# Performance work log

Hardware: AMD Instinct MI355X
Metric: run time of the kernel (lower is better)

## Reference

```python
import jax, jax.numpy as jnp
import numpy as np

B, T, D = 4, 2048, 1024
H, HD = 16, 64  # num_heads, head_size; H*HD == D
DFF = 4 * D
EPS = 1e-5

def _ln(x, g, b):
    mu = jnp.mean(x, axis=-1, keepdims=True)
    var = jnp.mean(jnp.square(x - mu), axis=-1, keepdims=True)
    return (x - mu) * jax.lax.rsqrt(var + EPS) * g + b

def setup_inputs() -> dict:
    key = jax.random.key(0)
    ks = jax.random.split(key, 12)
    s = lambda fan_in: 1.0 / np.sqrt(fan_in)
    return {
        "x": jax.random.normal(ks[0], (B, T, D), jnp.float32),
        "Wq": jax.random.normal(ks[1], (H, D, HD), jnp.float32) * s(D),
        "Wk": jax.random.normal(ks[2], (H, D, HD), jnp.float32) * s(D),
        "Wv": jax.random.normal(ks[3], (H, D, HD), jnp.float32) * s(D),
        "Wo": jax.random.normal(ks[4], (D, D), jnp.float32) * s(D),
        "bo": jax.random.normal(ks[5], (D,), jnp.float32) * 0.01,
        "W1": jax.random.normal(ks[6], (D, DFF), jnp.float32) * s(D),
        "b1": jax.random.normal(ks[7], (DFF,), jnp.float32) * 0.01,
        "W2": jax.random.normal(ks[8], (DFF, D), jnp.float32) * s(DFF),
        "b2": jax.random.normal(ks[9], (D,), jnp.float32) * 0.01,
        "g1": jnp.ones((D,), jnp.float32),
        "be1": jnp.zeros((D,), jnp.float32),
        "g2": jnp.ones((D,), jnp.float32),
        "be2": jnp.zeros((D,), jnp.float32),
    }

def reference(x, Wq, Wk, Wv, Wo, bo, W1, b1, W2, b2, g1, be1, g2, be2):
    # pre-LN attention
    h = _ln(x, g1, be1)                                   # [B,T,D]
    q = jnp.einsum('btd,hde->bhte', h, Wq)                # [B,H,T,HD]
    k = jnp.einsum('btd,hde->bhte', h, Wk)
    v = jnp.einsum('btd,hde->bhte', h, Wv)
    scores = jnp.einsum('bhte,bhse->bhts', q, k) * (HD ** -0.5)  # [B,H,T,T]
    mask = jnp.tril(jnp.ones((T, T), bool))
    scores = jnp.where(mask, scores, -jnp.inf)
    attn = jax.nn.softmax(scores, axis=-1)
    ctx = jnp.einsum('bhts,bhse->bhte', attn, v)          # [B,H,T,HD]
    ctx = ctx.transpose(0, 2, 1, 3).reshape(B, T, D)      # concat heads
    x = x + jnp.einsum('btd,de->bte', ctx, Wo) + bo
    # pre-LN FFN
    h2 = _ln(x, g2, be2)
    ff = jax.nn.relu(jnp.einsum('btd,df->btf', h2, W1) + b1)
    x = x + jnp.einsum('btf,fd->btd', ff, W2) + b2
    return x
```

## Files before the change

### kernel.cpp

```cpp
#include <hip/hip_runtime.h>
#include <stdint.h>

#define B_ 4
#define T_ 2048
#define D_ 1024
#define H_ 16
#define HD_ 64
#define DFF_ 4096
#define M_ (B_ * T_)

typedef __bf16 bf16x8 __attribute__((ext_vector_type(8)));
typedef float f32x4 __attribute__((ext_vector_type(4)));

__device__ __forceinline__ uint16_t f2bf(float f) {
  union { float f; uint32_t u; } v;
  v.f = f;
  uint32_t r = v.u + 0x7FFF + ((v.u >> 16) & 1);
  return (uint16_t)(r >> 16);
}

#define GLD_LDS(gp, lp)                                                        \
  __builtin_amdgcn_global_load_lds(                                            \
      (const __attribute__((address_space(1))) void*)(gp),                     \
      (__attribute__((address_space(3))) void*)(lp), 16, 0, 0)

__global__ __launch_bounds__(256) void ln_bf16(const float* __restrict__ x,
                                               const float* __restrict__ gamma,
                                               const float* __restrict__ beta,
                                               uint16_t* __restrict__ out) {
  __shared__ float red[4];
  const int tid = threadIdx.x;
  const size_t row = blockIdx.x;
  const float4 v = ((const float4*)(x + row * D_))[tid];
  float s = v.x + v.y + v.z + v.w;
#pragma unroll
  for (int off = 32; off >= 1; off >>= 1) s += __shfl_xor(s, off, 64);
  if ((tid & 63) == 0) red[tid >> 6] = s;
  __syncthreads();
  const float mean = (red[0] + red[1] + red[2] + red[3]) * (1.0f / D_);
  const float d0 = v.x - mean, d1 = v.y - mean, d2 = v.z - mean, d3 = v.w - mean;
  float ss = d0 * d0 + d1 * d1 + d2 * d2 + d3 * d3;
#pragma unroll
  for (int off = 32; off >= 1; off >>= 1) ss += __shfl_xor(ss, off, 64);
  __syncthreads();
  if ((tid & 63) == 0) red[tid >> 6] = ss;
  __syncthreads();
  const float var = (red[0] + red[1] + red[2] + red[3]) * (1.0f / D_);
  const float rstd = rsqrtf(var + 1e-5f);
  const float4 g = ((const float4*)gamma)[tid];
  const float4 b = ((const float4*)beta)[tid];
  ushort4 o;
  o.x = f2bf(d0 * rstd * g.x + b.x);
  o.y = f2bf(d1 * rstd * g.y + b.y);
  o.z = f2bf(d2 * rstd * g.z + b.z);
  o.w = f2bf(d3 * rstd * g.w + b.w);
  ((ushort4*)(out + row * D_))[tid] = o;
}

__global__ __launch_bounds__(256) void prep_weights(
    const float* __restrict__ Wq, const float* __restrict__ Wk,
    const float* __restrict__ Wv, const float* __restrict__ Wo,
    const float* __restrict__ W1, const float* __restrict__ W2,
    uint16_t* __restrict__ wqkvt, uint16_t* __restrict__ wot,
    uint16_t* __restrict__ w1t, uint16_t* __restrict__ w2t) {
  __shared__ float tile[32][33];
  const int tx = threadIdx.x & 31, ty = threadIdx.x >> 5;
  const int pid = blockIdx.x;

  if (pid >= 9216) {
    const int p = pid - 9216;
    const int bx = p & 1, by = (p >> 1) & 31, z = p >> 6;
    const int which = z >> 4, hh = z & 15;
    const float* W = (which == 0) ? Wq : ((which == 1) ? Wk : Wv);
    const float* in = W + (size_t)hh * D_ * HD_;
    const int e0 = bx * 32, d0 = by * 32;
#pragma unroll
    for (int i = 0; i < 32; i += 8)
      tile[ty + i][tx] = in[(size_t)(d0 + ty + i) * HD_ + e0 + tx];
    __syncthreads();
#pragma unroll
    for (int i = 0; i < 32; i += 8)
      wqkvt[((size_t)(which * 1024 + hh * 64) + e0 + ty + i) * D_ + d0 + tx] =
          f2bf(tile[tx][ty + i]);
    return;
  }

  const float* in;
  uint16_t* out;
  int R, C, bx, by;
  if (pid < 1024) {
    in = Wo; out = wot; R = 1024; C = 1024; bx = pid & 31; by = pid >> 5;
  } else if (pid < 5120) {
    const int p = pid - 1024;
    in = W1; out = w1t; R = 1024; C = 4096; bx = p & 127; by = p >> 7;
  } else {
    const int p = pid - 5120;
    in = W2; out = w2t; R = 4096; C = 1024; bx = p & 31; by = p >> 5;
  }
  const int c0 = bx * 32, r0 = by * 32;
#pragma unroll
  for (int i = 0; i < 32; i += 8)
    tile[ty + i][tx] = in[(size_t)(r0 + ty + i) * C + c0 + tx];
  __syncthreads();
#pragma unroll
  for (int i = 0; i < 32; i += 8)
    out[(size_t)(c0 + ty + i) * R + r0 + tx] = f2bf(tile[tx][ty + i]);
}

template <int BN>
__global__ __launch_bounds__(256) void gemm_bf16(const uint16_t* __restrict__ A,
                                                 const uint16_t* __restrict__ Bt,
                                                 void* __restrict__ C,
                                                 const float* __restrict__ bias,
                                                 const float* __restrict__ resid,
                                                 int M, int N, int K, int lda,
                                                 int ldb, int flags) {
  constexpr int NJ = BN / 32;
  __shared__ __align__(16) uint16_t As[128 * 64];
  __shared__ __align__(16) uint16_t Bs[BN * 64];
  const int tid = threadIdx.x;
  const int lane = tid & 63, w = tid >> 6;
  const int quad = lane >> 4, lr = lane & 15;
  const int wr = w >> 1, wc = w & 1;

  const int n_tiles = N / BN;
  const int pid = blockIdx.x;
  const int grp = 16 * n_tiles;
  const int gid = pid / grp;
  const int rem = pid - gid * grp;
  const int nt = rem / 16;
  const int mt = gid * 16 + (rem - nt * 16);
  const int bn0 = nt * BN, bm0 = mt * 128;

  f32x4 acc[4][NJ];
#pragma unroll
  for (int i = 0; i < 4; i++)
#pragma unroll
    for (int j = 0; j < NJ; j++) acc[i][j] = f32x4{0.f, 0.f, 0.f, 0.f};

  const int s_row = lane >> 3, s_slot = lane & 7;

  for (int k0 = 0; k0 < K; k0 += 64) {
#pragma unroll
    for (int u = 0; u < 4; u++) {
      const int r = w * 32 + u * 8 + s_row;
      const int cg = s_slot ^ (r & 7);
      GLD_LDS(A + (size_t)(bm0 + r) * lda + k0 + cg * 8, As + (w * 32 + u * 8) * 64);
    }
#pragma unroll
    for (int u = 0; u < NJ; u++) {
      const int r = w * (BN / 4) + u * 8 + s_row;
      const int cg = s_slot ^ (r & 7);
      GLD_LDS(Bt + (size_t)(bn0 + r) * ldb + k0 + cg * 8,
              Bs + (w * (BN / 4) + u * 8) * 64);
    }
    __syncthreads();

#pragma unroll
    for (int ks = 0; ks < 2; ks++) {
      bf16x8 af[4], bfr[NJ];
#pragma unroll
      for (int i = 0; i < 4; i++) {
        const int m = wr * 64 + i * 16 + lr;
        const int slot = (ks * 4 + quad) ^ (m & 7);
        af[i] = *(const bf16x8*)(As + m * 64 + slot * 8);
      }
#pragma unroll
      for (int j = 0; j < NJ; j++) {
        const int n = wc * (BN / 2) + j * 16 + lr;
        const int slot = (ks * 4 + quad) ^ (n & 7);
        bfr[j] = *(const bf16x8*)(Bs + n * 64 + slot * 8);
      }
#pragma unroll
      for (int i = 0; i < 4; i++)
#pragma unroll
        for (int j = 0; j < NJ; j++)
          acc[i][j] =
              __builtin_amdgcn_mfma_f32_16x16x32_bf16(af[i], bfr[j], acc[i][j], 0, 0, 0);
    }
    __syncthreads();
  }

  const int base_m = bm0 + wr * 64 + quad * 4;
  const int base_n = bn0 + wc * (BN / 2) + lr;
#pragma unroll
  for (int i = 0; i < 4; i++) {
#pragma unroll
    for (int j = 0; j < NJ; j++) {
      const int col = base_n + j * 16;
      const float bv = bias ? bias[col] : 0.f;
#pragma unroll
      for (int r = 0; r < 4; r++) {
        const size_t row = base_m + i * 16 + r;
        float v = acc[i][j][r] + bv;
        if (resid) v += resid[row * N + col];
        if (flags & 1) v = fmaxf(v, 0.f);
        if (flags & 2)
          ((uint16_t*)C)[row * N + col] = f2bf(v);
        else
          ((float*)C)[row * N + col] = v;
      }
    }
  }
}

__global__ __launch_bounds__(256) void v_transpose(const uint16_t* __restrict__ qkv,
                                                   uint16_t* __restrict__ vtb) {
  __shared__ __align__(16) uint16_t tile[64 * 72];
  const int tid = threadIdx.x;
  const int t0 = blockIdx.x * 64;
  const int bh = blockIdx.y;
  const int b = bh >> 4, h = bh & 15;
  const uint16_t* src = qkv + (size_t)b * T_ * 3072 + 2048 + h * 64;
#pragma unroll
  for (int u = 0; u < 2; u++) {
    const int uu = tid + u * 256;
    const int r = uu >> 3, c = uu & 7;
    *(int4*)(tile + r * 72 + c * 8) =
        *(const int4*)(src + (size_t)(t0 + r) * 3072 + c * 8);
  }
  __syncthreads();
  uint16_t* dst = vtb + ((size_t)bh * 64) * T_ + t0;
#pragma unroll
  for (int u = 0; u < 2; u++) {
    const int uu = tid + u * 256;
    const int e = uu >> 3, c2 = uu & 7;
    union { uint16_t u16[8]; int4 v; } tmp;
#pragma unroll
    for (int jj = 0; jj < 8; jj++) tmp.u16[jj] = tile[(c2 * 8 + jj) * 72 + e];
    *(int4*)(dst + (size_t)e * T_ + c2 * 8) = tmp.v;
  }
}

__global__ __launch_bounds__(256) void attn_mfma(const uint16_t* __restrict__ qkv,
                                                 const uint16_t* __restrict__ vtb,
                                                 uint16_t* __restrict__ ctx) {
  __shared__ __align__(16) uint16_t Ks[2][64 * 64];
  __shared__ __align__(16) uint16_t Vt[2][64 * 64];
  __shared__ __align__(16) uint16_t Ps[128 * 72];
  const int tid = threadIdx.x;
  const int lane = tid & 63, w = tid >> 6;
  const int quad = lane >> 4, lr = lane & 15;
  const int lr7 = lr & 7;
  const int h = blockIdx.y, b = blockIdx.z;
  const uint16_t* base = qkv + (size_t)b * T_ * 3072 + h * 64;
  const uint16_t* vbase = vtb + ((size_t)(b * H_ + h) * 64) * T_;
  const int s_row = lane >> 3, s_slot = lane & 7;

#pragma unroll
  for (int half = 0; half < 2; half++) {
    const int tq = (half == 0) ? (int)blockIdx.x : 15 - (int)blockIdx.x;
    const int q0 = tq * 128;

    bf16x8 aq[2][2];
#pragma unroll
    for (int i = 0; i < 2; i++)
#pragma unroll
      for (int ks = 0; ks < 2; ks++)
        aq[i][ks] = *(const bf16x8*)(base + (size_t)(q0 + w * 32 + i * 16 + lr) * 3072 +
                                     ks * 32 + quad * 8);

    f32x4 oacc[2][4];
#pragma unroll
    for (int i = 0; i < 2; i++)
#pragma unroll
      for (int j = 0; j < 4; j++) oacc[i][j] = f32x4{0.f, 0.f, 0.f, 0.f};
    float l_part[2] = {0.f, 0.f};

    const int row_min_w = q0 + w * 32;
    const int row_max_w = row_min_w + 31;
    const int nstg = 2 * tq + 2;

    __syncthreads();
#pragma unroll
    for (int u = 0; u < 2; u++) {
      const int r = w * 16 + u * 8 + s_row;
      const int cg = s_slot ^ (r & 7);
      GLD_LDS(base + 1024 + (size_t)r * 3072 + cg * 8, Ks[0] + (w * 16 + u * 8) * 64);
      GLD_LDS(vbase + (size_t)r * T_ + cg * 8, Vt[0] + (w * 16 + u * 8) * 64);
    }

    for (int st = 0; st < nstg; st++) {
      __syncthreads();
      if (st + 1 < nstg) {
        uint16_t* Kb = Ks[(st + 1) & 1];
        uint16_t* Vb = Vt[(st + 1) & 1];
#pragma unroll
        for (int u = 0; u < 2; u++) {
          const int r = w * 16 + u * 8 + s_row;
          const int cg = s_slot ^ (r & 7);
          GLD_LDS(base + 1024 + (size_t)((st + 1) * 64 + r) * 3072 + cg * 8,
                  Kb + (w * 16 + u * 8) * 64);
          GLD_LDS(vbase + (size_t)r * T_ + (st + 1) * 64 + cg * 8,
                  Vb + (w * 16 + u * 8) * 64);
        }
      }

      if (st * 64 > row_max_w) continue;
      const uint16_t* Kb = Ks[st & 1];
      const uint16_t* Vb = Vt[st & 1];

      f32x4 sa[2][4];
#pragma unroll
      for (int i = 0; i < 2; i++)
#pragma unroll
        for (int sf = 0; sf < 4; sf++) sa[i][sf] = f32x4{0.f, 0.f, 0.f, 0.f};
#pragma unroll
      for (int ks = 0; ks < 2; ks++) {
        bf16x8 ak[4];
#pragma unroll
        for (int sf = 0; sf < 4; sf++) {
          const int slot = (ks * 4 + quad) ^ lr7;
          ak[sf] = *(const bf16x8*)(Kb + (sf * 16 + lr) * 64 + slot * 8);
        }
#pragma unroll
        for (int i = 0; i < 2; i++)
#pragma unroll
          for (int sf = 0; sf < 4; sf++)
            sa[i][sf] = __builtin_amdgcn_mfma_f32_16x16x32_bf16(ak[sf], aq[i][ks],
                                                                sa[i][sf], 0, 0, 0);
      }

      const bool diag = (st * 64 + 63 > row_min_w);
      if (diag) {
#pragma unroll
        for (int i = 0; i < 2; i++) {
          const int mrow = q0 + w * 32 + i * 16 + lr;
#pragma unroll
          for (int sf = 0; sf < 4; sf++) {
            const int s0 = st * 64 + sf * 16 + quad * 4;
            float p[4];
#pragma unroll
            for (int r = 0; r < 4; r++) {
              float sv = sa[i][sf][r];
              if (s0 + r > mrow) sv = -1e30f;
              p[r] = exp2f(fmaf(sv, 0.18033688f, -28.8539008f));
              l_part[i] += p[r];
            }
            ushort4 pk;
            pk.x = f2bf(p[0]);
            pk.y = f2bf(p[1]);
            pk.z = f2bf(p[2]);
            pk.w = f2bf(p[3]);
            *(ushort4*)(Ps + (size_t)(w * 32 + i * 16 + lr) * 72 + sf * 16 + quad * 4) =
                pk;
          }
        }
      } else {
#pragma unroll
        for (int i = 0; i < 2; i++) {
#pragma unroll
          for (int sf = 0; sf < 4; sf++) {
            float p[4];
#pragma unroll
            for (int r = 0; r < 4; r++) {
              p[r] = exp2f(fmaf(sa[i][sf][r], 0.18033688f, -28.8539008f));
              l_part[i] += p[r];
            }
            ushort4 pk;
            pk.x = f2bf(p[0]);
            pk.y = f2bf(p[1]);
            pk.z = f2bf(p[2]);
            pk.w = f2bf(p[3]);
            *(ushort4*)(Ps + (size_t)(w * 32 + i * 16 + lr) * 72 + sf * 16 + quad * 4) =
                pk;
          }
        }
      }

#pragma unroll
      for (int ks = 0; ks < 2; ks++) {
        bf16x8 ap[2], bv[4];
#pragma unroll
        for (int i = 0; i < 2; i++)
          ap[i] = *(const bf16x8*)(Ps + (size_t)(w * 32 + i * 16 + lr) * 72 + ks * 32 +
                                   quad * 8);
#pragma unroll
        for (int j = 0; j < 4; j++) {
          const int slot = (ks * 4 + quad) ^ lr7;
          bv[j] = *(const bf16x8*)(Vb + (j * 16 + lr) * 64 + slot * 8);
        }
#pragma unroll
        for (int i = 0; i < 2; i++)
#pragma unroll
          for (int j = 0; j < 4; j++)
            oacc[i][j] =
                __builtin_amdgcn_mfma_f32_16x16x32_bf16(ap[i], bv[j], oacc[i][j], 0, 0, 0);
      }
    }

    float linv[2];
#pragma unroll
    for (int i = 0; i < 2; i++) {
      float l = l_part[i];
      l += __shfl_xor(l, 16, 64);
      l += __shfl_xor(l, 32, 64);
      linv[i] = 1.f / l;
    }
    uint16_t* ob =
        ctx + ((size_t)b * T_ + q0 + w * 32 + quad * 4) * D_ + h * 64 + lr;
#pragma unroll
    for (int i = 0; i < 2; i++)
#pragma unroll
      for (int r = 0; r < 4; r++) {
        const float inv = __shfl(linv[i], quad * 4 + r, 64);
#pragma unroll
        for (int j = 0; j < 4; j++)
          ob[(size_t)(i * 16 + r) * D_ + j * 16] = f2bf(oacc[i][j][r] * inv);
      }
  }
}

extern "C" void kernel_launch(void* const* d_in, const int* in_sizes, int n_in,
                              void* d_out, int out_size, void* d_ws, size_t ws_size,
                              hipStream_t stream) {
  const float* x = (const float*)d_in[0];
  const float* Wq = (const float*)d_in[1];
  const float* Wk = (const float*)d_in[2];
  const float* Wv = (const float*)d_in[3];
  const float* Wo = (const float*)d_in[4];
  const float* bo = (const float*)d_in[5];
  const float* W1 = (const float*)d_in[6];
  const float* b1 = (const float*)d_in[7];
  const float* W2 = (const float*)d_in[8];
  const float* b2 = (const float*)d_in[9];
  const float* g1 = (const float*)d_in[10];
  const float* be1 = (const float*)d_in[11];
  const float* g2 = (const float*)d_in[12];
  const float* be2 = (const float*)d_in[13];
  float* out = (float*)d_out;

  const size_t MB = 1024ull * 1024ull;
  if (ws_size < 200 * MB) return;
  char* ws = (char*)d_ws;
  uint16_t* hbuf = (uint16_t*)(ws + 0 * MB);
  uint16_t* wqkvt = (uint16_t*)(ws + 16 * MB);
  uint16_t* wot = (uint16_t*)(ws + 22 * MB);
  uint16_t* w1t = (uint16_t*)(ws + 24 * MB);
  uint16_t* w2t = (uint16_t*)(ws + 32 * MB);
  float* x1 = (float*)(ws + 40 * MB);
  uint16_t* qkvb = (uint16_t*)(ws + 72 * MB);
  uint16_t* ctxb = (uint16_t*)(ws + 120 * MB);
  uint16_t* vtb = (uint16_t*)(ws + 136 * MB);
  uint16_t* ffb = (uint16_t*)(ws + 136 * MB);

  prep_weights<<<12288, 256, 0, stream>>>(Wq, Wk, Wv, Wo, W1, W2, wqkvt, wot, w1t,
                                          w2t);
  ln_bf16<<<M_, 256, 0, stream>>>(x, g1, be1, hbuf);
  gemm_bf16<128><<<64 * 24, 256, 0, stream>>>(hbuf, wqkvt, qkvb, nullptr, nullptr,
                                              M_, 3 * D_, D_, D_, D_, 2);
  v_transpose<<<dim3(T_ / 64, B_ * H_), 256, 0, stream>>>(qkvb, vtb);
  attn_mfma<<<dim3(8, H_, B_), 256, 0, stream>>>(qkvb, vtb, ctxb);
  gemm_bf16<64><<<64 * 16, 256, 0, stream>>>(ctxb, wot, x1, bo, x, M_, D_, D_, D_,
                                             D_, 0);
  ln_bf16<<<M_, 256, 0, stream>>>(x1, g2, be2, hbuf);
  gemm_bf16<128><<<64 * 32, 256, 0, stream>>>(hbuf, w1t, ffb, b1, nullptr, M_, DFF_,
                                              D_, D_, D_, 1 | 2);
  gemm_bf16<64><<<64 * 16, 256, 0, stream>>>(ffb, w2t, out, b2, x1, M_, D_, DFF_,
                                             DFF_, DFF_, 0);
}
```

Baseline: 552.7 us.

## Process both query tiles per K/V stage to share tile loads

The attention kernel now handles its two paired query tiles (tq and 15-tq) together in a single pass over the K/V stages, so each K/V tile is loaded into LDS once and reused by both query tiles instead of being loaded again for each half. The shared compute is moved into a helper function. The double-buffered prefetch is replaced by a single buffer with a load, barrier, compute sequence, which drops the overlap of global loads with compute. It also doubles the accumulator and query register state, which raises register pressure and may lower occupancy.

Result: no change. 546.7 us (-1.1%).

```diff
diff --git a/kernel.cpp b/kernel.cpp
--- a/kernel.cpp
+++ b/kernel.cpp
@@ -232,163 +232,166 @@
   }
 }
 
+__device__ __forceinline__ void attn_tile_compute(
+    const uint16_t* __restrict__ Kb, const uint16_t* __restrict__ Vb,
+    uint16_t* __restrict__ Ps, const bf16x8 (&aq)[2][2], f32x4 (&oacc)[2][4],
+    float (&l_part)[2], int st, int q0, int w, int quad, int lr) {
+  const int lr7 = lr & 7;
+  const int row_min_w = q0 + w * 32;
+
+  f32x4 sa[2][4];
+#pragma unroll
+  for (int i = 0; i < 2; i++)
+#pragma unroll
+    for (int sf = 0; sf < 4; sf++) sa[i][sf] = f32x4{0.f, 0.f, 0.f, 0.f};
+#pragma unroll
+  for (int ks = 0; ks < 2; ks++) {
+    bf16x8 ak[4];
+#pragma unroll
+    for (int sf = 0; sf < 4; sf++) {
+      const int slot = (ks * 4 + quad) ^ lr7;
+      ak[sf] = *(const bf16x8*)(Kb + (sf * 16 + lr) * 64 + slot * 8);
+    }
+#pragma unroll
+    for (int i = 0; i < 2; i++)
+#pragma unroll
+      for (int sf = 0; sf < 4; sf++)
+        sa[i][sf] =
+            __builtin_amdgcn_mfma_f32_16x16x32_bf16(ak[sf], aq[i][ks], sa[i][sf], 0, 0, 0);
+  }
+
+  const bool diag = (st * 64 + 63 > row_min_w);
+  if (diag) {
+#pragma unroll
+    for (int i = 0; i < 2; i++) {
+      const int mrow = q0 + w * 32 + i * 16 + lr;
+#pragma unroll
+      for (int sf = 0; sf < 4; sf++) {
+        const int s0 = st * 64 + sf * 16 + quad * 4;
+        float p[4];
+#pragma unroll
+        for (int r = 0; r < 4; r++) {
+          float sv = sa[i][sf][r];
+          if (s0 + r > mrow) sv = -1e30f;
+          p[r] = exp2f(fmaf(sv, 0.18033688f, -28.8539008f));
+          l_part[i] += p[r];
+        }
+        ushort4 pk;
+        pk.x = f2bf(p[0]);
+        pk.y = f2bf(p[1]);
+        pk.z = f2bf(p[2]);
+        pk.w = f2bf(p[3]);
+        *(ushort4*)(Ps + (size_t)(w * 32 + i * 16 + lr) * 72 + sf * 16 + quad * 4) = pk;
+      }
+    }
+  } else {
+#pragma unroll
+    for (int i = 0; i < 2; i++) {
+#pragma unroll
+      for (int sf = 0; sf < 4; sf++) {
+        float p[4];
+#pragma unroll
+        for (int r = 0; r < 4; r++) {
+          p[r] = exp2f(fmaf(sa[i][sf][r], 0.18033688f, -28.8539008f));
+          l_part[i] += p[r];
+        }
+        ushort4 pk;
+        pk.x = f2bf(p[0]);
+        pk.y = f2bf(p[1]);
+        pk.z = f2bf(p[2]);
+        pk.w = f2bf(p[3]);
+        *(ushort4*)(Ps + (size_t)(w * 32 + i * 16 + lr) * 72 + sf * 16 + quad * 4) = pk;
+      }
+    }
+  }
+
+#pragma unroll
+  for (int ks = 0; ks < 2; ks++) {
+    bf16x8 ap[2], bv[4];
+#pragma unroll
+    for (int i = 0; i < 2; i++)
+      ap[i] = *(const bf16x8*)(Ps + (size_t)(w * 32 + i * 16 + lr) * 72 + ks * 32 +
+                               quad * 8);
+#pragma unroll
+    for (int j = 0; j < 4; j++) {
+      const int slot = (ks * 4 + quad) ^ lr7;
+      bv[j] = *(const bf16x8*)(Vb + (j * 16 + lr) * 64 + slot * 8);
+    }
+#pragma unroll
+    for (int i = 0; i < 2; i++)
+#pragma unroll
+      for (int j = 0; j < 4; j++)
+        oacc[i][j] =
+            __builtin_amdgcn_mfma_f32_16x16x32_bf16(ap[i], bv[j], oacc[i][j], 0, 0, 0);
+  }
+}
+
 __global__ __launch_bounds__(256) void attn_mfma(const uint16_t* __restrict__ qkv,
                                                  const uint16_t* __restrict__ vtb,
                                                  uint16_t* __restrict__ ctx) {
-  __shared__ __align__(16) uint16_t Ks[2][64 * 64];
-  __shared__ __align__(16) uint16_t Vt[2][64 * 64];
+  __shared__ __align__(16) uint16_t Ks[64 * 64];
+  __shared__ __align__(16) uint16_t Vt[64 * 64];
   __shared__ __align__(16) uint16_t Ps[128 * 72];
   const int tid = threadIdx.x;
   const int lane = tid & 63, w = tid >> 6;
   const int quad = lane >> 4, lr = lane & 15;
-  const int lr7 = lr & 7;
   const int h = blockIdx.y, b = blockIdx.z;
   const uint16_t* base = qkv + (size_t)b * T_ * 3072 + h * 64;
   const uint16_t* vbase = vtb + ((size_t)(b * H_ + h) * 64) * T_;
   const int s_row = lane >> 3, s_slot = lane & 7;
 
-#pragma unroll
-  for (int half = 0; half < 2; half++) {
-    const int tq = (half == 0) ? (int)blockIdx.x : 15 - (int)blockIdx.x;
-    const int q0 = tq * 128;
-
-    bf16x8 aq[2][2];
-#pragma unroll
-    for (int i = 0; i < 2; i++)
-#pragma unroll
-      for (int ks = 0; ks < 2; ks++)
-        aq[i][ks] = *(const bf16x8*)(base + (size_t)(q0 + w * 32 + i * 16 + lr) * 3072 +
-                                     ks * 32 + quad * 8);
-
-    f32x4 oacc[2][4];
-#pragma unroll
-    for (int i = 0; i < 2; i++)
-#pragma unroll
-      for (int j = 0; j < 4; j++) oacc[i][j] = f32x4{0.f, 0.f, 0.f, 0.f};
-    float l_part[2] = {0.f, 0.f};
-
-    const int row_min_w = q0 + w * 32;
-    const int row_max_w = row_min_w + 31;
-    const int nstg = 2 * tq + 2;
-
+  const int tqA = blockIdx.x, tqB = 15 - tqA;
+  const int q0A = tqA * 128, q0B = tqB * 128;
+  const int nstgA = 2 * tqA + 2, nstgB = 2 * tqB + 2;
+  const int nstg = (nstgA > nstgB) ? nstgA : nstgB;
+
+  bf16x8 aqA[2][2], aqB[2][2];
+#pragma unroll
+  for (int i = 0; i < 2; i++)
+#pragma unroll
+    for (int ks = 0; ks < 2; ks++) {
+      aqA[i][ks] = *(const bf16x8*)(base + (size_t)(q0A + w * 32 + i * 16 + lr) * 3072 +
+                                    ks * 32 + quad * 8);
+      aqB[i][ks] = *(const bf16x8*)(base + (size_t)(q0B + w * 32 + i * 16 + lr) * 3072 +
+                                    ks * 32 + quad * 8);
+    }
+
+  f32x4 oaccA[2][4], oaccB[2][4];
+#pragma unroll
+  for (int i = 0; i < 2; i++)
+#pragma unroll
+    for (int j = 0; j < 4; j++) {
+      oaccA[i][j] = f32x4{0.f, 0.f, 0.f, 0.f};
+      oaccB[i][j] = f32x4{0.f, 0.f, 0.f, 0.f};
+    }
+  float lA[2] = {0.f, 0.f}, lB[2] = {0.f, 0.f};
+
+  const int row_maxA = q0A + w * 32 + 31;
+  const int row_maxB = q0B + w * 32 + 31;
+
+  for (int st = 0; st < nstg; st++) {
     __syncthreads();
 #pragma unroll
     for (int u = 0; u < 2; u++) {
       const int r = w * 16 + u * 8 + s_row;
       const int cg = s_slot ^ (r & 7);
-      GLD_LDS(base + 1024 + (size_t)r * 3072 + cg * 8, Ks[0] + (w * 16 + u * 8) * 64);
-      GLD_LDS(vbase + (size_t)r * T_ + cg * 8, Vt[0] + (w * 16 + u * 8) * 64);
-    }
-
-    for (int st = 0; st < nstg; st++) {
-      __syncthreads();
-      if (st + 1 < nstg) {
-        uint16_t* Kb = Ks[(st + 1) & 1];
-        uint16_t* Vb = Vt[(st + 1) & 1];
-#pragma unroll
-        for (int u = 0; u < 2; u++) {
-          const int r = w * 16 + u * 8 + s_row;
-          const int cg = s_slot ^ (r & 7);
-          GLD_LDS(base + 1024 + (size_t)((st + 1) * 64 + r) * 3072 + cg * 8,
-                  Kb + (w * 16 + u * 8) * 64);
-          GLD_LDS(vbase + (size_t)r * T_ + (st + 1) * 64 + cg * 8,
-                  Vb + (w * 16 + u * 8) * 64);
-        }
-      }
-
-      if (st * 64 > row_max_w) continue;
-      const uint16_t* Kb = Ks[st & 1];
-      const uint16_t* Vb = Vt[st & 1];
-
-      f32x4 sa[2][4];
-#pragma unroll
-      for (int i = 0; i < 2; i++)
-#pragma unroll
-        for (int sf = 0; sf < 4; sf++) sa[i][sf] = f32x4{0.f, 0.f, 0.f, 0.f};
-#pragma unroll
-      for (int ks = 0; ks < 2; ks++) {
-        bf16x8 ak[4];
-#pragma unroll
-        for (int sf = 0; sf < 4; sf++) {
-          const int slot = (ks * 4 + quad) ^ lr7;
-          ak[sf] = *(const bf16x8*)(Kb + (sf * 16 + lr) * 64 + slot * 8);
-        }
-#pragma unroll
-        for (int i = 0; i < 2; i++)
-#pragma unroll
-          for (int sf = 0; sf < 4; sf++)
-            sa[i][sf] = __builtin_amdgcn_mfma_f32_16x16x32_bf16(ak[sf], aq[i][ks],
-                                                                sa[i][sf], 0, 0, 0);
-      }
-
-      const bool diag = (st * 64 + 63 > row_min_w);
-      if (diag) {
-#pragma unroll
-        for (int i = 0; i < 2; i++) {
-          const int mrow = q0 + w * 32 + i * 16 + lr;
-#pragma unroll
-          for (int sf = 0; sf < 4; sf++) {
-            const int s0 = st * 64 + sf * 16 + quad * 4;
-            float p[4];
-#pragma unroll
-            for (int r = 0; r < 4; r++) {
-              float sv = sa[i][sf][r];
-              if (s0 + r > mrow) sv = -1e30f;
-              p[r] = exp2f(fmaf(sv, 0.18033688f, -28.8539008f));
-              l_part[i] += p[r];
-            }
-            ushort4 pk;
-            pk.x = f2bf(p[0]);
-            pk.y = f2bf(p[1]);
-            pk.z = f2bf(p[2]);
-            pk.w = f2bf(p[3]);
-            *(ushort4*)(Ps + (size_t)(w * 32 + i * 16 + lr) * 72 + sf * 16 + quad * 4) =
-                pk;
-          }
-        }
-      } else {
-#pragma unroll
-        for (int i = 0; i < 2; i++) {
-#pragma unroll
-          for (int sf = 0; sf < 4; sf++) {
-            float p[4];
-#pragma unroll
-            for (int r = 0; r < 4; r++) {
-              p[r] = exp2f(fmaf(sa[i][sf][r], 0.18033688f, -28.8539008f));
-              l_part[i] += p[r];
-            }
-            ushort4 pk;
-            pk.x = f2bf(p[0]);
-            pk.y = f2bf(p[1]);
-            pk.z = f2bf(p[2]);
-            pk.w = f2bf(p[3]);
-            *(ushort4*)(Ps + (size_t)(w * 32 + i * 16 + lr) * 72 + sf * 16 + quad * 4) =
-                pk;
-          }
-        }
-      }
-
-#pragma unroll
-      for (int ks = 0; ks < 2; ks++) {
-        bf16x8 ap[2], bv[4];
-#pragma unroll
-        for (int i = 0; i < 2; i++)
-          ap[i] = *(const bf16x8*)(Ps + (size_t)(w * 32 + i * 16 + lr) * 72 + ks * 32 +
-                                   quad * 8);
-#pragma unroll
-        for (int j = 0; j < 4; j++) {
-          const int slot = (ks * 4 + quad) ^ lr7;
-          bv[j] = *(const bf16x8*)(Vb + (j * 16 + lr) * 64 + slot * 8);
-        }
-#pragma unroll
-        for (int i = 0; i < 2; i++)
-#pragma unroll
-          for (int j = 0; j < 4; j++)
-            oacc[i][j] =
-                __builtin_amdgcn_mfma_f32_16x16x32_bf16(ap[i], bv[j], oacc[i][j], 0, 0, 0);
-      }
-    }
-
+      GLD_LDS(base + 1024 + (size_t)(st * 64 + r) * 3072 + cg * 8,
+              Ks + (w * 16 + u * 8) * 64);
+      GLD_LDS(vbase + (size_t)r * T_ + st * 64 + cg * 8, Vt + (w * 16 + u * 8) * 64);
+    }
+    __syncthreads();
+
+    if (st < nstgA && st * 64 <= row_maxA)
+      attn_tile_compute(Ks, Vt, Ps, aqA, oaccA, lA, st, q0A, w, quad, lr);
+    if (st < nstgB && st * 64 <= row_maxB)
+      attn_tile_compute(Ks, Vt, Ps, aqB, oaccB, lB, st, q0B, w, quad, lr);
+  }
+
+#pragma unroll
+  for (int half = 0; half < 2; half++) {
+    const int q0 = half ? q0B : q0A;
+    f32x4(&oacc)[2][4] = half ? oaccB : oaccA;
+    float* l_part = half ? lB : lA;
     float linv[2];
 #pragma unroll
     for (int i = 0; i < 2; i++) {
```
